# Kernel tuning notes

Measured on AMD Instinct MI355X. Metric: run time of the kernel, lower is better.

The kernel has to match this reference:

```python
import jax, jax.numpy as jnp
import numpy as np
import math

N, T, D, H = 64, 512, 1024, 1024

def setup_inputs() -> dict:
    key = jax.random.key(0)
    k1, k2, k3, k4 = jax.random.split(key, 4)
    x = jax.random.normal(k1, (N, T, D), dtype=jnp.float32)
    h0 = jax.random.normal(k2, (N, H), dtype=jnp.float32)
    Wx = jax.random.normal(k3, (D, 4 * H), dtype=jnp.float32) / math.sqrt(D)
    Wh = jax.random.normal(k4, (H, 4 * H), dtype=jnp.float32) / math.sqrt(H)
    b = jnp.zeros((4 * H,), dtype=jnp.float32)
    return {"x": x, "h0": h0, "Wx": Wx, "Wh": Wh, "b": b}

def reference(x, h0, Wx, Wh, b):
    Hdim = h0.shape[1]
    c0 = jnp.zeros_like(h0)
    # Precompute input projection for all timesteps: [N,T,4H] -> time-major [T,N,4H]
    xW = jnp.einsum('ntd,dk->tnk', x, Wx) + b

    def step(carry, xw_t):
        prev_h, prev_c = carry
        a = xw_t + prev_h @ Wh  # [N, 4H]
        i = jax.nn.sigmoid(a[:, :Hdim])
        f = jax.nn.sigmoid(a[:, Hdim:2 * Hdim])
        o = jax.nn.sigmoid(a[:, 2 * Hdim:3 * Hdim])
        g = jnp.tanh(a[:, 3 * Hdim:])
        next_c = f * prev_c + i * g
        next_h = o * jnp.tanh(next_c)
        return (next_h, next_c), next_h

    _, hs = jax.lax.scan(step, (h0, c0), xW)  # hs: [T, N, H]
    return jnp.transpose(hs, (1, 0, 2))  # [N, T, H]
```

## Files before the change

### kernel.cpp

```cpp
#include <hip/hip_runtime.h>

typedef short bf16x8 __attribute__((ext_vector_type(8)));
typedef float f32x4 __attribute__((ext_vector_type(4)));

static constexpr int kT = 512;
static constexpr int kN = 64;
static constexpr int kD = 1024;
static constexpr int kH = 1024;
static constexpr int kG = 4 * kH;

__device__ __forceinline__ unsigned short f2bf(float f) {
  unsigned u = __builtin_bit_cast(unsigned, f);
  return (unsigned short)((u + 0x7fffu + ((u >> 16) & 1u)) >> 16);
}
__device__ __forceinline__ unsigned pack2(float a, float b) {
  return (unsigned)f2bf(a) | ((unsigned)f2bf(b) << 16);
}
__device__ __forceinline__ float fsigmoid(float v) {
  return __builtin_amdgcn_rcpf(1.0f + __expf(-v));
}
__device__ __forceinline__ float ftanh(float v) {
  return 1.0f - 2.0f * __builtin_amdgcn_rcpf(__expf(2.0f * v) + 1.0f);
}

__device__ __forceinline__ bf16x8 gld16_coh(unsigned long long a) {
  bf16x8 r;
  asm volatile("global_load_dwordx4 %0, %1, off sc0 sc1" : "=v"(r) : "v"(a) : "memory");
  return r;
}
__device__ __forceinline__ bf16x8 gld16(unsigned long long a) {
  bf16x8 r;
  asm volatile("global_load_dwordx4 %0, %1, off" : "=v"(r) : "v"(a) : "memory");
  return r;
}

__global__ __launch_bounds__(256) void xconv(const float* __restrict__ x,
                                             unsigned short* __restrict__ xbf) {
  const int gid = blockIdx.x * 256 + threadIdx.x;
  const float4* x4 = (const float4*)x;
  uint4* o = (uint4*)xbf;
  for (int i = gid; i < (kN * kT * kD) / 8; i += 2048 * 256) {
    const float4 f0 = x4[2 * i];
    const float4 f1 = x4[2 * i + 1];
    uint4 p;
    p.x = pack2(f0.x, f0.y); p.y = pack2(f0.z, f0.w);
    p.z = pack2(f1.x, f1.y); p.w = pack2(f1.z, f1.w);
    o[i] = p;
  }
}

template <bool PRE>
__global__ __launch_bounds__(256, 1)
void lstm_persistent(const float* __restrict__ x, const float* __restrict__ h0,
                     const float* __restrict__ Wx, const float* __restrict__ Wh,
                     const float* __restrict__ bias, float* __restrict__ out,
                     unsigned short* __restrict__ hbuf, unsigned int* __restrict__ cnt,
                     const unsigned short* __restrict__ xbf) {
  __shared__ float ps[16 * 320];

  const int tid = threadIdx.x;
  const int bx = blockIdx.x;
  const int dom = (bx & 7) >> 1;
  const int ug = ((bx >> 3) << 1) | (bx & 1);
  const int wv = tid >> 6;
  const int lane = tid & 63;

  const int colc = ug * 16 + (lane & 15);
  const int krow = (lane >> 4) * 8;
  const int kb = wv * 256;
  bf16x8 wxf[4][8], whf[4][8];
#pragma unroll
  for (int ct = 0; ct < 4; ++ct) {
#pragma unroll
    for (int ks = 0; ks < 8; ++ks) {
      bf16x8 vx, vh;
#pragma unroll
      for (int e = 0; e < 8; ++e) {
        const size_t k = (size_t)(kb + ks * 32 + krow + e);
        vx[e] = (short)f2bf(Wx[k * kG + ct * kH + colc]);
        vh[e] = (short)f2bf(Wh[k * kG + ct * kH + colc]);
      }
      wxf[ct][ks] = vx;
      whf[ct][ks] = vh;
    }
  }

  const int n_l = tid >> 4;
  const int j_l = tid & 15;
  const int jg = ug * 16 + j_l;
  const float b_i = bias[jg];
  const float b_f = bias[kH + jg];
  const float b_o = bias[2 * kH + jg];
  const float b_g = bias[3 * kH + jg];
  float c = 0.0f;

  const int arow = lane & 15;
  const int nrow = dom * 16 + arow;
  const unsigned long long xbase0 =
      (unsigned long long)nrow * kT * kD * 2 + (unsigned long long)(kb + krow) * 2;
  const unsigned long long hbase0 =
      (unsigned long long)nrow * kH * 2 + (unsigned long long)(kb + krow) * 2;

  unsigned int* mycnt = cnt + (size_t)(dom * 64 + ug) * 32;
  unsigned int* dcnt = cnt + (size_t)dom * 64 * 32;
  unsigned int* dflag = cnt + 8192 + (size_t)dom * 32;
  const bool is_agg = (ug == 0) && (wv == 0);

  bf16x8 xfrag[8], hfrag[8];

  if (PRE) {
    const unsigned long long xb = (unsigned long long)xbf + xbase0;
#pragma unroll
    for (int ks = 0; ks < 8; ++ks) xfrag[ks] = gld16(xb + (unsigned)(ks * 64));
  } else {
    const float* xr = x + (size_t)nrow * kT * kD + (kb + krow);
#pragma unroll
    for (int ks = 0; ks < 8; ++ks) {
      const float4 f0 = *(const float4*)(xr + ks * 32);
      const float4 f1 = *(const float4*)(xr + ks * 32 + 4);
      bf16x8 v;
      v[0] = (short)f2bf(f0.x); v[1] = (short)f2bf(f0.y);
      v[2] = (short)f2bf(f0.z); v[3] = (short)f2bf(f0.w);
      v[4] = (short)f2bf(f1.x); v[5] = (short)f2bf(f1.y);
      v[6] = (short)f2bf(f1.z); v[7] = (short)f2bf(f1.w);
      xfrag[ks] = v;
    }
  }
  {
    const float* hr = h0 + (size_t)nrow * kH + (kb + krow);
#pragma unroll
    for (int ks = 0; ks < 8; ++ks) {
      const float4 f0 = *(const float4*)(hr + ks * 32);
      const float4 f1 = *(const float4*)(hr + ks * 32 + 4);
      bf16x8 v;
      v[0] = (short)f2bf(f0.x); v[1] = (short)f2bf(f0.y);
      v[2] = (short)f2bf(f0.z); v[3] = (short)f2bf(f0.w);
      v[4] = (short)f2bf(f1.x); v[5] = (short)f2bf(f1.y);
      v[6] = (short)f2bf(f1.z); v[7] = (short)f2bf(f1.w);
      hfrag[ks] = v;
    }
  }
  asm volatile("s_waitcnt vmcnt(0)" ::: "memory");
  __builtin_amdgcn_sched_barrier(0);

  f32x4 acc[4];
#pragma unroll
  for (int ct = 0; ct < 4; ++ct) acc[ct] = (f32x4){0.f, 0.f, 0.f, 0.f};
#pragma unroll
  for (int ks = 0; ks < 8; ++ks)
#pragma unroll
    for (int ct = 0; ct < 4; ++ct)
      acc[ct] = __builtin_amdgcn_mfma_f32_16x16x32_bf16(xfrag[ks], wxf[ct][ks], acc[ct], 0, 0, 0);

  for (int t = 0; t < kT; ++t) {
    asm volatile("s_waitcnt vmcnt(4)" ::: "memory");
    __builtin_amdgcn_sched_barrier(0);
#pragma unroll
    for (int ks = 0; ks < 4; ++ks)
#pragma unroll
      for (int ct = 0; ct < 4; ++ct)
        acc[ct] = __builtin_amdgcn_mfma_f32_16x16x32_bf16(hfrag[ks], whf[ct][ks], acc[ct], 0, 0, 0);
    asm volatile("s_waitcnt vmcnt(0)" ::: "memory");
    __builtin_amdgcn_sched_barrier(0);
#pragma unroll
    for (int ks = 4; ks < 8; ++ks)
#pragma unroll
      for (int ct = 0; ct < 4; ++ct)
        acc[ct] = __builtin_amdgcn_mfma_f32_16x16x32_bf16(hfrag[ks], whf[ct][ks], acc[ct], 0, 0, 0);

#pragma unroll
    for (int ct = 0; ct < 4; ++ct) {
      const int o = (ct * 4 + wv) * 320 + (lane & 15) * 20 + (lane >> 4) * 4;
      *(f32x4*)&ps[o] = acc[ct];
    }
    __syncthreads();

    float a4[4];
#pragma unroll
    for (int g = 0; g < 4; ++g) {
      a4[g] = ps[(g * 4 + 0) * 320 + j_l * 20 + n_l]
            + ps[(g * 4 + 1) * 320 + j_l * 20 + n_l]
            + ps[(g * 4 + 2) * 320 + j_l * 20 + n_l]
            + ps[(g * 4 + 3) * 320 + j_l * 20 + n_l];
    }
    const float gi = fsigmoid(a4[0] + b_i);
    const float gf = fsigmoid(a4[1] + b_f);
    const float go = fsigmoid(a4[2] + b_o);
    const float gg = ftanh(a4[3] + b_g);
    c = gf * c + gi * gg;
    const float hv = go * ftanh(c);

    if (t < kT - 1) {
      const unsigned mybf = (unsigned)f2bf(hv);
      const unsigned up = (unsigned)__shfl_xor((int)mybf, 1);
      if ((j_l & 1) == 0) {
        const size_t eidx = (size_t)((t + 1) & 1) * (kN * kH) +
                            (size_t)(dom * 16 + n_l) * kH + (size_t)(ug * 16 + j_l);
        __hip_atomic_store((unsigned*)(hbuf + eidx), mybf | (up << 16),
                           __ATOMIC_RELAXED, __HIP_MEMORY_SCOPE_AGENT);
      }
      asm volatile("s_waitcnt vmcnt(0)" ::: "memory");
      __builtin_amdgcn_sched_barrier(0);
      if (lane == 0)
        __hip_atomic_fetch_add(mycnt, 1u, __ATOMIC_RELAXED, __HIP_MEMORY_SCOPE_AGENT);

      __builtin_nontemporal_store(hv, &out[((size_t)(dom * 16 + n_l) * kT + t) * kH + jg]);

      if (PRE) {
        const unsigned long long xb = (unsigned long long)xbf + xbase0 +
                                      (unsigned long long)(t + 1) * 2048u;
#pragma unroll
        for (int ks = 0; ks < 8; ++ks) xfrag[ks] = gld16(xb + (unsigned)(ks * 64));
        asm volatile("s_waitcnt vmcnt(0)" ::: "memory");
        __builtin_amdgcn_sched_barrier(0);
      } else {
        const float* xr = x + (size_t)nrow * kT * kD + (size_t)(t + 1) * kD + (kb + krow);
#pragma unroll
        for (int ks = 0; ks < 8; ++ks) {
          const float4 f0 = *(const float4*)(xr + ks * 32);
          const float4 f1 = *(const float4*)(xr + ks * 32 + 4);
          bf16x8 v;
          v[0] = (short)f2bf(f0.x); v[1] = (short)f2bf(f0.y);
          v[2] = (short)f2bf(f0.z); v[3] = (short)f2bf(f0.w);
          v[4] = (short)f2bf(f1.x); v[5] = (short)f2bf(f1.y);
          v[6] = (short)f2bf(f1.z); v[7] = (short)f2bf(f1.w);
          xfrag[ks] = v;
        }
      }
#pragma unroll
      for (int ct = 0; ct < 4; ++ct) acc[ct] = (f32x4){0.f, 0.f, 0.f, 0.f};
#pragma unroll
      for (int ks = 0; ks < 8; ++ks)
#pragma unroll
        for (int ct = 0; ct < 4; ++ct)
          acc[ct] = __builtin_amdgcn_mfma_f32_16x16x32_bf16(xfrag[ks], wxf[ct][ks], acc[ct], 0, 0, 0);

      const unsigned tgt = (unsigned)(t + 1);
      if (is_agg) {
        for (;;) {
          unsigned v = __hip_atomic_load(dcnt + lane * 32, __ATOMIC_RELAXED,
                                         __HIP_MEMORY_SCOPE_AGENT);
#pragma unroll
          for (int s = 1; s < 64; s <<= 1) v += (unsigned)__shfl_xor((int)v, s);
          if (v >= 256u * tgt) break;
          __builtin_amdgcn_s_sleep(1);
        }
        if (lane == 0)
          __hip_atomic_store(dflag, tgt, __ATOMIC_RELAXED, __HIP_MEMORY_SCOPE_AGENT);
      } else if (lane == 0) {
        while (__hip_atomic_load(dflag, __ATOMIC_RELAXED, __HIP_MEMORY_SCOPE_AGENT) < tgt)
          __builtin_amdgcn_s_sleep(1);
      }
      asm volatile("" ::: "memory");
      __builtin_amdgcn_sched_barrier(0);

      const unsigned long long hb = (unsigned long long)hbuf +
                                    (unsigned long long)((t + 1) & 1) * (kN * kH * 2) +
                                    hbase0;
#pragma unroll
      for (int ks = 0; ks < 8; ++ks) hfrag[ks] = gld16_coh(hb + (unsigned)(ks * 64));
    } else {
      __builtin_nontemporal_store(hv, &out[((size_t)(dom * 16 + n_l) * kT + t) * kH + jg]);
    }
  }
}

extern "C" void kernel_launch(void* const* d_in, const int* in_sizes, int n_in,
                              void* d_out, int out_size, void* d_ws, size_t ws_size,
                              hipStream_t stream) {
  (void)in_sizes; (void)n_in; (void)out_size;
  const float* x  = (const float*)d_in[0];
  const float* h0 = (const float*)d_in[1];
  const float* Wx = (const float*)d_in[2];
  const float* Wh = (const float*)d_in[3];
  const float* b  = (const float*)d_in[4];
  float* out = (float*)d_out;

  unsigned int* cnt = (unsigned int*)d_ws;
  unsigned short* hbuf = (unsigned short*)((char*)d_ws + 36864);
  unsigned short* xbf = (unsigned short*)((char*)d_ws + 36864 + (size_t)2 * kN * kH * 2);
  const size_t need_pre = 36864 + (size_t)2 * kN * kH * 2 + (size_t)kN * kT * kD * 2;

  hipMemsetAsync(d_ws, 0, 36864, stream);

  if (ws_size >= need_pre) {
    hipLaunchKernelGGL(xconv, dim3(2048), dim3(256), 0, stream, x, xbf);
    hipLaunchKernelGGL(HIP_KERNEL_NAME(lstm_persistent<true>), dim3(256), dim3(256),
                       0, stream, x, h0, Wx, Wh, b, out, hbuf, cnt, xbf);
  } else {
    hipLaunchKernelGGL(HIP_KERNEL_NAME(lstm_persistent<false>), dim3(256), dim3(256),
                       0, stream, x, h0, Wx, Wh, b, out, hbuf, cnt,
                       (const unsigned short*)nullptr);
  }
}
```

Baseline: 2.477 ms.

## Hoist input projection into a separate bulk GEMM and slim the recurrent kernel

```diff
diff --git a/kernel.cpp b/kernel.cpp
--- a/kernel.cpp
+++ b/kernel.cpp
@@ -49,6 +49,267 @@
   }
 }
 
+__global__ __launch_bounds__(256) void h0conv(const float* __restrict__ h0,
+                                              unsigned short* __restrict__ hbuf) {
+  const int gid = blockIdx.x * 256 + threadIdx.x;
+  const float4 f0 = ((const float4*)h0)[2 * gid];
+  const float4 f1 = ((const float4*)h0)[2 * gid + 1];
+  uint4 p;
+  p.x = pack2(f0.x, f0.y); p.y = pack2(f0.z, f0.w);
+  p.z = pack2(f1.x, f1.y); p.w = pack2(f1.z, f1.w);
+  ((uint4*)hbuf)[gid] = p;
+}
+
+__global__ __launch_bounds__(256) void wconv(const float* __restrict__ Wx,
+                                             unsigned short* __restrict__ wxt) {
+  __shared__ float T[64][65];
+  const int k0 = (blockIdx.x >> 6) * 64;
+  const int c0 = (blockIdx.x & 63) * 64;
+  const int r = threadIdx.x >> 6;
+  const int cc = threadIdx.x & 63;
+#pragma unroll
+  for (int i = 0; i < 16; ++i)
+    T[r + i * 4][cc] = Wx[(size_t)(k0 + r + i * 4) * kG + c0 + cc];
+  __syncthreads();
+#pragma unroll
+  for (int i = 0; i < 16; ++i) {
+    const int orow = r + i * 4;
+    wxt[(size_t)(c0 + orow) * kD + k0 + cc] = f2bf(T[cc][orow]);
+  }
+}
+
+template <bool XF32>
+__global__ __launch_bounds__(256, 2)
+void xw_gemm(const unsigned short* __restrict__ A, const unsigned short* __restrict__ Bt,
+             void* __restrict__ Cout) {
+  __shared__ unsigned short As[128 * 64];
+  __shared__ unsigned short Bs[128 * 64];
+  const int tid = threadIdx.x;
+  const int lane = tid & 63, wv = tid >> 6;
+  const int m0 = (blockIdx.x >> 5) * 128;
+  const int n0 = (blockIdx.x & 31) * 128;
+  const int wm = wv >> 1, wn = wv & 1;
+
+  f32x4 acc[4][4];
+#pragma unroll
+  for (int mi = 0; mi < 4; ++mi)
+#pragma unroll
+    for (int ni = 0; ni < 4; ++ni) acc[mi][ni] = (f32x4){0.f, 0.f, 0.f, 0.f};
+
+  for (int kk = 0; kk < kD; kk += 64) {
+    uint4 av[4], bv[4];
+#pragma unroll
+    for (int q = 0; q < 4; ++q) {
+      const int c = q * 256 + tid;
+      const int row = c >> 3;
+      const int so = ((c & 7) * 16) ^ ((row & 7) << 4);
+      av[q] = *(const uint4*)((const char*)A + (size_t)(m0 + row) * 2048 + kk * 2 + so);
+      bv[q] = *(const uint4*)((const char*)Bt + (size_t)(n0 + row) * 2048 + kk * 2 + so);
+    }
+    __syncthreads();
+#pragma unroll
+    for (int q = 0; q < 4; ++q) {
+      const int c = q * 256 + tid;
+      *(uint4*)((char*)As + c * 16) = av[q];
+      *(uint4*)((char*)Bs + c * 16) = bv[q];
+    }
+    __syncthreads();
+#pragma unroll
+    for (int s = 0; s < 2; ++s) {
+      bf16x8 af[4], bfr[4];
+#pragma unroll
+      for (int i = 0; i < 4; ++i) {
+        const int ar = wm * 64 + i * 16 + (lane & 15);
+        af[i] = *(const bf16x8*)((const char*)As + ar * 128 +
+                                 ((s * 64 + (lane >> 4) * 16) ^ ((ar & 7) << 4)));
+        const int bc = wn * 64 + i * 16 + (lane & 15);
+        bfr[i] = *(const bf16x8*)((const char*)Bs + bc * 128 +
+                                  ((s * 64 + (lane >> 4) * 16) ^ ((bc & 7) << 4)));
+      }
+#pragma unroll
+      for (int mi = 0; mi < 4; ++mi)
+#pragma unroll
+        for (int ni = 0; ni < 4; ++ni)
+          acc[mi][ni] = __builtin_amdgcn_mfma_f32_16x16x32_bf16(af[mi], bfr[ni], acc[mi][ni], 0, 0, 0);
+    }
+  }
+#pragma unroll
+  for (int mi = 0; mi < 4; ++mi)
+#pragma unroll
+    for (int ni = 0; ni < 4; ++ni) {
+      const int col = n0 + wn * 64 + ni * 16 + (lane & 15);
+#pragma unroll
+      for (int r = 0; r < 4; ++r) {
+        const size_t row = (size_t)(m0 + wm * 64 + mi * 16 + (lane >> 4) * 4 + r);
+        if (XF32)
+          __builtin_nontemporal_store(acc[mi][ni][r], (float*)Cout + row * kG + col);
+        else
+          __builtin_nontemporal_store(f2bf(acc[mi][ni][r]),
+                                      (unsigned short*)Cout + row * kG + col);
+      }
+    }
+}
+
+template <bool XF32>
+__global__ __launch_bounds__(256, 1)
+void lstm_rec(const float* __restrict__ Wh, const float* __restrict__ bias,
+              const void* __restrict__ xW, float* __restrict__ out,
+              unsigned short* __restrict__ hbuf, unsigned int* __restrict__ cnt) {
+  __shared__ float ps[32 * 320];
+
+  const int tid = threadIdx.x;
+  const int bx = blockIdx.x;
+  const int dom = bx & 7;
+  const int j = bx >> 3;
+  const int wv = tid >> 6;
+  const int lane = tid & 63;
+
+  const int kb = wv * 256;
+  const int krow = (lane >> 4) * 8;
+  const int lcol = lane & 15;
+  bf16x8 whf[8][8];
+#pragma unroll
+  for (int ct = 0; ct < 8; ++ct) {
+    const int gcol = (ct >> 1) * kH + j * 32 + (ct & 1) * 16 + lcol;
+#pragma unroll
+    for (int ks = 0; ks < 8; ++ks) {
+      bf16x8 v;
+#pragma unroll
+      for (int e = 0; e < 8; ++e)
+        v[e] = (short)f2bf(Wh[(size_t)(kb + ks * 32 + krow + e) * kG + gcol]);
+      whf[ct][ks] = v;
+    }
+  }
+
+  const int n_l = tid >> 5;
+  const int jj = tid & 31;
+  const int hcol = j * 32 + jj;
+  const float b0 = bias[hcol];
+  const float b1 = bias[kH + hcol];
+  const float b2 = bias[2 * kH + hcol];
+  const float b3 = bias[3 * kH + hcol];
+  float c = 0.0f;
+
+  const int nrow = dom * 8 + (lane & 7);
+  const unsigned long long hrow0 =
+      (unsigned long long)hbuf + ((unsigned long long)nrow * kH + kb + krow) * 2;
+
+  unsigned int* myflag = cnt + (size_t)bx * 32;
+  unsigned int* polladdr = cnt + (size_t)(((lane & 31) * 8 + dom)) * 32;
+
+  const unsigned* xw32 = (const unsigned*)xW;
+  const unsigned short* xw16 = (const unsigned short*)xW;
+  const size_t xrow0 = (size_t)(dom * 8 + n_l) * kT;
+
+  unsigned xr0, xr1, xr2, xr3;
+  {
+    const size_t e0 = xrow0 * (size_t)kG + (size_t)hcol;
+    if (XF32) {
+      xr0 = xw32[e0];          xr1 = xw32[e0 + kH];
+      xr2 = xw32[e0 + 2 * kH]; xr3 = xw32[e0 + 3 * kH];
+    } else {
+      xr0 = xw16[e0];          xr1 = xw16[e0 + kH];
+      xr2 = xw16[e0 + 2 * kH]; xr3 = xw16[e0 + 3 * kH];
+    }
+  }
+  bf16x8 hfrag[8];
+#pragma unroll
+  for (int ks = 0; ks < 8; ++ks) hfrag[ks] = gld16_coh(hrow0 + (unsigned)(ks * 64));
+
+  for (int t = 0; t < kT; ++t) {
+    f32x4 acc[8];
+#pragma unroll
+    for (int ct = 0; ct < 8; ++ct) acc[ct] = (f32x4){0.f, 0.f, 0.f, 0.f};
+
+    asm volatile("s_waitcnt vmcnt(4)" ::: "memory");
+    __builtin_amdgcn_sched_barrier(0);
+#pragma unroll
+    for (int ks = 0; ks < 4; ++ks)
+#pragma unroll
+      for (int ct = 0; ct < 8; ++ct)
+        acc[ct] = __builtin_amdgcn_mfma_f32_16x16x32_bf16(hfrag[ks], whf[ct][ks], acc[ct], 0, 0, 0);
+    asm volatile("s_waitcnt vmcnt(0)" ::: "memory");
+    __builtin_amdgcn_sched_barrier(0);
+#pragma unroll
+    for (int ks = 4; ks < 8; ++ks)
+#pragma unroll
+      for (int ct = 0; ct < 8; ++ct)
+        acc[ct] = __builtin_amdgcn_mfma_f32_16x16x32_bf16(hfrag[ks], whf[ct][ks], acc[ct], 0, 0, 0);
+
+#pragma unroll
+    for (int ct = 0; ct < 8; ++ct)
+      *(f32x4*)&ps[(ct * 4 + wv) * 320 + (lane & 15) * 20 + (lane >> 4) * 4] = acc[ct];
+    __syncthreads();
+
+    float a4[4];
+#pragma unroll
+    for (int g = 0; g < 4; ++g) {
+      const int ctb = (g * 2 + (jj >> 4)) * 4;
+      const int cw = (jj & 15) * 20 + n_l;
+      a4[g] = ps[(ctb + 0) * 320 + cw] + ps[(ctb + 1) * 320 + cw]
+            + ps[(ctb + 2) * 320 + cw] + ps[(ctb + 3) * 320 + cw];
+    }
+    const float xv0 = __builtin_bit_cast(float, XF32 ? xr0 : (xr0 << 16));
+    const float xv1 = __builtin_bit_cast(float, XF32 ? xr1 : (xr1 << 16));
+    const float xv2 = __builtin_bit_cast(float, XF32 ? xr2 : (xr2 << 16));
+    const float xv3 = __builtin_bit_cast(float, XF32 ? xr3 : (xr3 << 16));
+    const float gi = fsigmoid(a4[0] + xv0 + b0);
+    const float gf = fsigmoid(a4[1] + xv1 + b1);
+    const float go = fsigmoid(a4[2] + xv2 + b2);
+    const float gg = ftanh(a4[3] + xv3 + b3);
+    c = gf * c + gi * gg;
+    const float hv = go * ftanh(c);
+
+    if (t < kT - 1) {
+      const int buf1 = (t + 1) & 1;
+      const unsigned mybf = (unsigned)f2bf(hv);
+      const unsigned up = (unsigned)__shfl_xor((int)mybf, 1);
+      if ((jj & 1) == 0) {
+        const size_t eidx = (size_t)buf1 * (kN * kH) +
+                            (size_t)(dom * 8 + n_l) * kH + (size_t)hcol;
+        __hip_atomic_store((unsigned*)(hbuf + eidx), mybf | (up << 16),
+                           __ATOMIC_RELAXED, __HIP_MEMORY_SCOPE_AGENT);
+      }
+      asm volatile("s_waitcnt vmcnt(0)" ::: "memory");
+      __syncthreads();
+
+      if (tid == 0)
+        __hip_atomic_store(myflag, (unsigned)(t + 1),
+                           __ATOMIC_RELAXED, __HIP_MEMORY_SCOPE_AGENT);
+
+      __builtin_nontemporal_store(hv, &out[(xrow0 + t) * kH + hcol]);
+      {
+        const size_t e1 = (xrow0 + t + 1) * (size_t)kG + (size_t)hcol;
+        if (XF32) {
+          xr0 = xw32[e1];          xr1 = xw32[e1 + kH];
+          xr2 = xw32[e1 + 2 * kH]; xr3 = xw32[e1 + 3 * kH];
+        } else {
+          xr0 = xw16[e1];          xr1 = xw16[e1 + kH];
+          xr2 = xw16[e1 + 2 * kH]; xr3 = xw16[e1 + 3 * kH];
+        }
+      }
+
+      if (wv == 0) {
+        const int tgt = t + 1;
+        for (;;) {
+          unsigned v = __hip_atomic_load(polladdr, __ATOMIC_RELAXED,
+                                         __HIP_MEMORY_SCOPE_AGENT);
+          if (__all((int)v >= tgt)) break;
+          __builtin_amdgcn_s_sleep(2);
+        }
+      }
+      __syncthreads();
+      __builtin_amdgcn_sched_barrier(0);
+
+      const unsigned long long hb = hrow0 + (unsigned long long)buf1 * (kN * kH * 2);
+#pragma unroll
+      for (int ks = 0; ks < 8; ++ks) hfrag[ks] = gld16_coh(hb + (unsigned)(ks * 64));
+    } else {
+      __builtin_nontemporal_store(hv, &out[(xrow0 + t) * kH + hcol]);
+    }
+  }
+}
+
 template <bool PRE>
 __global__ __launch_bounds__(256, 1)
 void lstm_persistent(const float* __restrict__ x, const float* __restrict__ h0,
@@ -102,7 +363,6 @@
       (unsigned long long)nrow * kH * 2 + (unsigned long long)(kb + krow) * 2;
 
   unsigned int* mycnt = cnt + (size_t)(dom * 64 + ug) * 32;
-  unsigned int* dcnt = cnt + (size_t)dom * 64 * 32;
   unsigned int* dflag = cnt + 8192 + (size_t)dom * 32;
   const bool is_agg = (ug == 0) && (wv == 0);
 
@@ -238,8 +498,8 @@
       const unsigned tgt = (unsigned)(t + 1);
       if (is_agg) {
         for (;;) {
-          unsigned v = __hip_atomic_load(dcnt + lane * 32, __ATOMIC_RELAXED,
-                                         __HIP_MEMORY_SCOPE_AGENT);
+          unsigned v = __hip_atomic_load(cnt + (size_t)(dom * 64 + lane) * 32,
+                                         __ATOMIC_RELAXED, __HIP_MEMORY_SCOPE_AGENT);
 #pragma unroll
           for (int s = 1; s < 64; s <<= 1) v += (unsigned)__shfl_xor((int)v, s);
           if (v >= 256u * tgt) break;
@@ -276,14 +536,39 @@
   const float* b  = (const float*)d_in[4];
   float* out = (float*)d_out;
 
+  const size_t CNT = 36864;
+  const size_t o_hbuf = CNT;
+  const size_t o_xbf = o_hbuf + 262144;
+  const size_t o_wxt = o_xbf + 67108864;
+  const size_t o_xw = o_wxt + 8388608;
+  const size_t need_f32 = o_xw + (size_t)536870912;
+  const size_t need_b16 = o_xw + (size_t)268435456;
+
   unsigned int* cnt = (unsigned int*)d_ws;
-  unsigned short* hbuf = (unsigned short*)((char*)d_ws + 36864);
-  unsigned short* xbf = (unsigned short*)((char*)d_ws + 36864 + (size_t)2 * kN * kH * 2);
-  const size_t need_pre = 36864 + (size_t)2 * kN * kH * 2 + (size_t)kN * kT * kD * 2;
-
-  hipMemsetAsync(d_ws, 0, 36864, stream);
-
-  if (ws_size >= need_pre) {
+  unsigned short* hbuf = (unsigned short*)((char*)d_ws + o_hbuf);
+  unsigned short* xbf = (unsigned short*)((char*)d_ws + o_xbf);
+  unsigned short* wxt = (unsigned short*)((char*)d_ws + o_wxt);
+  void* xw = (void*)((char*)d_ws + o_xw);
+
+  hipMemsetAsync(d_ws, 0, CNT, stream);
+
+  if (ws_size >= need_b16) {
+    const bool f32p = (ws_size >= need_f32);
+    hipLaunchKernelGGL(h0conv, dim3(32), dim3(256), 0, stream, h0, hbuf);
+    hipLaunchKernelGGL(xconv, dim3(2048), dim3(256), 0, stream, x, xbf);
+    hipLaunchKernelGGL(wconv, dim3(1024), dim3(256), 0, stream, Wx, wxt);
+    if (f32p) {
+      hipLaunchKernelGGL(HIP_KERNEL_NAME(xw_gemm<true>), dim3(8192), dim3(256), 0, stream,
+                         xbf, wxt, xw);
+      hipLaunchKernelGGL(HIP_KERNEL_NAME(lstm_rec<true>), dim3(256), dim3(256), 0, stream,
+                         Wh, b, xw, out, hbuf, cnt);
+    } else {
+      hipLaunchKernelGGL(HIP_KERNEL_NAME(xw_gemm<false>), dim3(8192), dim3(256), 0, stream,
+                         xbf, wxt, xw);
+      hipLaunchKernelGGL(HIP_KERNEL_NAME(lstm_rec<false>), dim3(256), dim3(256), 0, stream,
+                         Wh, b, xw, out, hbuf, cnt);
+    }
+  } else if (ws_size >= o_wxt) {
     hipLaunchKernelGGL(xconv, dim3(2048), dim3(256), 0, stream, x, xbf);
     hipLaunchKernelGGL(HIP_KERNEL_NAME(lstm_persistent<true>), dim3(256), dim3(256),
                        0, stream, x, h0, Wx, Wh, b, out, hbuf, cnt, xbf);
```

New measurement: 3.352 ms. +35.3%, slower.

## Replace aggregator barrier with per-wave flags polled directly by each wave

Applied to the files above, without the earlier changes.

```diff
diff --git a/kernel.cpp b/kernel.cpp
--- a/kernel.cpp
+++ b/kernel.cpp
@@ -51,12 +51,12 @@
 
 template <bool PRE>
 __global__ __launch_bounds__(256, 1)
-void lstm_persistent(const float* __restrict__ x, const float* __restrict__ h0,
-                     const float* __restrict__ Wx, const float* __restrict__ Wh,
-                     const float* __restrict__ bias, float* __restrict__ out,
-                     unsigned short* __restrict__ hbuf, unsigned int* __restrict__ cnt,
-                     const unsigned short* __restrict__ xbf) {
-  __shared__ float ps[16 * 320];
+void lstm_fg(const float* __restrict__ x, const float* __restrict__ h0,
+             const float* __restrict__ Wx, const float* __restrict__ Wh,
+             const float* __restrict__ bias, float* __restrict__ out,
+             unsigned short* __restrict__ hbuf, unsigned* __restrict__ flags,
+             const unsigned short* __restrict__ xbf) {
+  __shared__ float ps[2][16 * 320];
 
   const int tid = threadIdx.x;
   const int bx = blockIdx.x;
@@ -100,11 +100,10 @@
       (unsigned long long)nrow * kT * kD * 2 + (unsigned long long)(kb + krow) * 2;
   const unsigned long long hbase0 =
       (unsigned long long)nrow * kH * 2 + (unsigned long long)(kb + krow) * 2;
-
-  unsigned int* mycnt = cnt + (size_t)(dom * 64 + ug) * 32;
-  unsigned int* dcnt = cnt + (size_t)dom * 64 * 32;
-  unsigned int* dflag = cnt + 8192 + (size_t)dom * 32;
-  const bool is_agg = (ug == 0) && (wv == 0);
+  const unsigned pubeidx = (unsigned)((dom * 16 + n_l) * kH + jg);
+
+  unsigned* myflag = flags + (dom * 256 + ug * 4 + wv);
+  unsigned* pollp = flags + (dom * 256 + wv * 64 + lane);
 
   bf16x8 xfrag[8], hfrag[8];
 
@@ -112,6 +111,8 @@
     const unsigned long long xb = (unsigned long long)xbf + xbase0;
 #pragma unroll
     for (int ks = 0; ks < 8; ++ks) xfrag[ks] = gld16(xb + (unsigned)(ks * 64));
+    asm volatile("s_waitcnt vmcnt(0)" ::: "memory");
+    __builtin_amdgcn_sched_barrier(0);
   } else {
     const float* xr = x + (size_t)nrow * kT * kD + (kb + krow);
 #pragma unroll
@@ -126,6 +127,14 @@
       xfrag[ks] = v;
     }
   }
+  f32x4 acc[4];
+#pragma unroll
+  for (int ct = 0; ct < 4; ++ct) acc[ct] = (f32x4){0.f, 0.f, 0.f, 0.f};
+#pragma unroll
+  for (int ks = 0; ks < 8; ++ks)
+#pragma unroll
+    for (int ct = 0; ct < 4; ++ct)
+      acc[ct] = __builtin_amdgcn_mfma_f32_16x16x32_bf16(xfrag[ks], wxf[ct][ks], acc[ct], 0, 0, 0);
   {
     const float* hr = h0 + (size_t)nrow * kH + (kb + krow);
 #pragma unroll
@@ -140,17 +149,6 @@
       hfrag[ks] = v;
     }
   }
-  asm volatile("s_waitcnt vmcnt(0)" ::: "memory");
-  __builtin_amdgcn_sched_barrier(0);
-
-  f32x4 acc[4];
-#pragma unroll
-  for (int ct = 0; ct < 4; ++ct) acc[ct] = (f32x4){0.f, 0.f, 0.f, 0.f};
-#pragma unroll
-  for (int ks = 0; ks < 8; ++ks)
-#pragma unroll
-    for (int ct = 0; ct < 4; ++ct)
-      acc[ct] = __builtin_amdgcn_mfma_f32_16x16x32_bf16(xfrag[ks], wxf[ct][ks], acc[ct], 0, 0, 0);
 
   for (int t = 0; t < kT; ++t) {
     asm volatile("s_waitcnt vmcnt(4)" ::: "memory");
@@ -168,20 +166,19 @@
       for (int ct = 0; ct < 4; ++ct)
         acc[ct] = __builtin_amdgcn_mfma_f32_16x16x32_bf16(hfrag[ks], whf[ct][ks], acc[ct], 0, 0, 0);
 
-#pragma unroll
-    for (int ct = 0; ct < 4; ++ct) {
-      const int o = (ct * 4 + wv) * 320 + (lane & 15) * 20 + (lane >> 4) * 4;
-      *(f32x4*)&ps[o] = acc[ct];
-    }
+    float* p = ps[t & 1];
+#pragma unroll
+    for (int ct = 0; ct < 4; ++ct)
+      *(f32x4*)&p[(ct * 4 + wv) * 320 + (lane & 15) * 20 + (lane >> 4) * 4] = acc[ct];
     __syncthreads();
 
     float a4[4];
 #pragma unroll
     for (int g = 0; g < 4; ++g) {
-      a4[g] = ps[(g * 4 + 0) * 320 + j_l * 20 + n_l]
-            + ps[(g * 4 + 1) * 320 + j_l * 20 + n_l]
-            + ps[(g * 4 + 2) * 320 + j_l * 20 + n_l]
-            + ps[(g * 4 + 3) * 320 + j_l * 20 + n_l];
+      a4[g] = p[(g * 4 + 0) * 320 + j_l * 20 + n_l]
+            + p[(g * 4 + 1) * 320 + j_l * 20 + n_l]
+            + p[(g * 4 + 2) * 320 + j_l * 20 + n_l]
+            + p[(g * 4 + 3) * 320 + j_l * 20 + n_l];
     }
     const float gi = fsigmoid(a4[0] + b_i);
     const float gf = fsigmoid(a4[1] + b_f);
@@ -191,18 +188,18 @@
     const float hv = go * ftanh(c);
 
     if (t < kT - 1) {
+      const unsigned tgt = (unsigned)(t + 1);
+      const unsigned buf1 = tgt & 1;
       const unsigned mybf = (unsigned)f2bf(hv);
       const unsigned up = (unsigned)__shfl_xor((int)mybf, 1);
       if ((j_l & 1) == 0) {
-        const size_t eidx = (size_t)((t + 1) & 1) * (kN * kH) +
-                            (size_t)(dom * 16 + n_l) * kH + (size_t)(ug * 16 + j_l);
-        __hip_atomic_store((unsigned*)(hbuf + eidx), mybf | (up << 16),
-                           __ATOMIC_RELAXED, __HIP_MEMORY_SCOPE_AGENT);
+        __hip_atomic_store((unsigned*)(hbuf + buf1 * (kN * kH) + pubeidx),
+                           mybf | (up << 16), __ATOMIC_RELAXED, __HIP_MEMORY_SCOPE_AGENT);
       }
       asm volatile("s_waitcnt vmcnt(0)" ::: "memory");
       __builtin_amdgcn_sched_barrier(0);
       if (lane == 0)
-        __hip_atomic_fetch_add(mycnt, 1u, __ATOMIC_RELAXED, __HIP_MEMORY_SCOPE_AGENT);
+        __hip_atomic_store(myflag, tgt, __ATOMIC_RELAXED, __HIP_MEMORY_SCOPE_AGENT);
 
       __builtin_nontemporal_store(hv, &out[((size_t)(dom * 16 + n_l) * kT + t) * kH + jg]);
 
@@ -235,28 +232,16 @@
         for (int ct = 0; ct < 4; ++ct)
           acc[ct] = __builtin_amdgcn_mfma_f32_16x16x32_bf16(xfrag[ks], wxf[ct][ks], acc[ct], 0, 0, 0);
 
-      const unsigned tgt = (unsigned)(t + 1);
-      if (is_agg) {
-        for (;;) {
-          unsigned v = __hip_atomic_load(dcnt + lane * 32, __ATOMIC_RELAXED,
-                                         __HIP_MEMORY_SCOPE_AGENT);
-#pragma unroll
-          for (int s = 1; s < 64; s <<= 1) v += (unsigned)__shfl_xor((int)v, s);
-          if (v >= 256u * tgt) break;
-          __builtin_amdgcn_s_sleep(1);
-        }
-        if (lane == 0)
-          __hip_atomic_store(dflag, tgt, __ATOMIC_RELAXED, __HIP_MEMORY_SCOPE_AGENT);
-      } else if (lane == 0) {
-        while (__hip_atomic_load(dflag, __ATOMIC_RELAXED, __HIP_MEMORY_SCOPE_AGENT) < tgt)
-          __builtin_amdgcn_s_sleep(1);
-      }
-      asm volatile("" ::: "memory");
+      for (;;) {
+        const unsigned v = __hip_atomic_load(pollp, __ATOMIC_RELAXED,
+                                             __HIP_MEMORY_SCOPE_AGENT);
+        if (__all((int)v >= (int)tgt)) break;
+        __builtin_amdgcn_s_sleep(1);
+      }
       __builtin_amdgcn_sched_barrier(0);
 
       const unsigned long long hb = (unsigned long long)hbuf +
-                                    (unsigned long long)((t + 1) & 1) * (kN * kH * 2) +
-                                    hbase0;
+                                    (unsigned long long)buf1 * (kN * kH * 2) + hbase0;
 #pragma unroll
       for (int ks = 0; ks < 8; ++ks) hfrag[ks] = gld16_coh(hb + (unsigned)(ks * 64));
     } else {
@@ -276,20 +261,23 @@
   const float* b  = (const float*)d_in[4];
   float* out = (float*)d_out;
 
-  unsigned int* cnt = (unsigned int*)d_ws;
-  unsigned short* hbuf = (unsigned short*)((char*)d_ws + 36864);
-  unsigned short* xbf = (unsigned short*)((char*)d_ws + 36864 + (size_t)2 * kN * kH * 2);
-  const size_t need_pre = 36864 + (size_t)2 * kN * kH * 2 + (size_t)kN * kT * kD * 2;
-
-  hipMemsetAsync(d_ws, 0, 36864, stream);
+  const size_t o_hbuf = 4096;
+  const size_t o_xbf = o_hbuf + 262144;
+  const size_t need_pre = o_xbf + (size_t)kN * kT * kD * 2;
+
+  unsigned* flags = (unsigned*)d_ws;
+  unsigned short* hbuf = (unsigned short*)((char*)d_ws + o_hbuf);
+  unsigned short* xbf = (unsigned short*)((char*)d_ws + o_xbf);
+
+  hipMemsetAsync(d_ws, 0, 4096, stream);
 
   if (ws_size >= need_pre) {
     hipLaunchKernelGGL(xconv, dim3(2048), dim3(256), 0, stream, x, xbf);
-    hipLaunchKernelGGL(HIP_KERNEL_NAME(lstm_persistent<true>), dim3(256), dim3(256),
-                       0, stream, x, h0, Wx, Wh, b, out, hbuf, cnt, xbf);
+    hipLaunchKernelGGL(HIP_KERNEL_NAME(lstm_fg<true>), dim3(256), dim3(256), 0, stream,
+                       x, h0, Wx, Wh, b, out, hbuf, flags, xbf);
   } else {
-    hipLaunchKernelGGL(HIP_KERNEL_NAME(lstm_persistent<false>), dim3(256), dim3(256),
-                       0, stream, x, h0, Wx, Wh, b, out, hbuf, cnt,
+    hipLaunchKernelGGL(HIP_KERNEL_NAME(lstm_fg<false>), dim3(256), dim3(256), 0, stream,
+                       x, h0, Wx, Wh, b, out, hbuf, flags,
                        (const unsigned short*)nullptr);
   }
 }
```

Result: faster. 2.011 ms (-18.8%).
